# Kernel optimization log

Hardware: AMD Instinct MI355X
Metric: run time of the kernel (lower is better)

## Reference

```python
import jax, jax.numpy as jnp
import numpy as np

# Module hyperparameters (init_kwargs)
NCE_K = 256      # samples per example (col 0 = positive)
NCE_T = 0.07     # temperature
EPS = 1e-7

# Problem sizes
B = 4096         # batch
D = 128          # embedding dim
N = 1_000_000    # memory bank size


def setup_inputs() -> dict:
    key = jax.random.key(0)
    k1, k2, k3, k4 = jax.random.split(key, 4)
    x = jax.random.normal(k1, (B, D), dtype=jnp.float32)
    targets = jax.random.randint(k2, (B,), 0, N)
    memory = jax.random.normal(k3, (N, D), dtype=jnp.float32) * 0.05
    # uniform multinomial-with-replacement sampling == uniform randint
    indices = jax.random.randint(k4, (B, NCE_K), 0, N)
    return {"x": x, "targets": targets, "memory": memory, "indices": indices}


def reference(x, targets, memory, indices):
    # nce_average: overwrite column 0 with the positive index
    idx = indices.at[:, 0].set(targets)              # [B, K]
    weight = memory[idx]                              # [B, K, D] gather
    logits = jnp.einsum('bkd,bd->bk', weight, x) / NCE_T
    sims = jnp.exp(logits)                            # [B, K]
    sims = sims / jnp.sum(sims, axis=1, keepdims=True) * (NCE_K / N)

    # NCE loss: K' = nce_k - 1 noise samples per example
    Kp = NCE_K - 1
    noise = Kp / N
    lnPmt = sims[:, 0] / (sims[:, 0] + noise + EPS)   # [B]
    lnPon = noise / (sims[:, 1:] + noise + EPS)       # [B, K-1]
    loss = -(jnp.log(lnPmt).mean() + jnp.log(lnPon).sum(axis=1).mean())
    return loss
```

## Files before the change

kernel.cpp:

```cpp
#include <hip/hip_runtime.h>

#define B_SZ 4096
#define D_SZ 128
#define K_SZ 256

constexpr float INV_T    = 1.0f / 0.07f;
constexpr float NOISE    = 255.0f / 1000000.0f;
constexpr float EPS_C    = 1e-7f;
constexpr float K_OVER_N = 256.0f / 1000000.0f;

__global__ __launch_bounds__(256, 8) void nce_main(
    const float* __restrict__ x,
    const int*   __restrict__ targets,
    const float* __restrict__ memory,
    const int*   __restrict__ indices,
    float*       __restrict__ partial)
{
    __shared__ float s_e[K_SZ];
    __shared__ float s_red[4];

    const int b    = blockIdx.x;
    const int tid  = threadIdx.x;
    const int lane = tid & 63;
    const int wave = tid >> 6;
    const int sub  = lane & 31;
    const int half = lane >> 5;

    const float4 xv = ((const float4*)(x + (size_t)b * D_SZ))[sub];

    const int myk = wave * 64 + lane;
    const int myidx = (myk == 0) ? targets[b]
                                 : indices[(size_t)b * K_SZ + myk];

    #pragma unroll 4
    for (int it = 0; it < 32; ++it) {
        const int kk  = it * 2 + half;
        const int row = __shfl(myidx, kk, 64);
        const float4 wv = ((const float4*)(memory + (size_t)row * D_SZ))[sub];
        float p = fmaf(wv.x, xv.x, fmaf(wv.y, xv.y,
                  fmaf(wv.z, xv.z, wv.w * xv.w)));
        #pragma unroll
        for (int m = 16; m >= 1; m >>= 1)
            p += __shfl_xor(p, m, 64);
        if (sub == 0)
            s_e[wave * 64 + kk] = expf(p * INV_T);
    }
    __syncthreads();

    const float e = s_e[tid];
    float sum = e;
    #pragma unroll
    for (int m = 32; m >= 1; m >>= 1)
        sum += __shfl_xor(sum, m, 64);
    if (lane == 0) s_red[wave] = sum;
    __syncthreads();
    const float S = s_red[0] + s_red[1] + s_red[2] + s_red[3];

    const float sims = e * (K_OVER_N / S);
    float term;
    if (tid == 0)
        term = logf(sims / (sims + NOISE + EPS_C));
    else
        term = logf(NOISE / (sims + NOISE + EPS_C));

    float t = term;
    #pragma unroll
    for (int m = 32; m >= 1; m >>= 1)
        t += __shfl_xor(t, m, 64);
    __syncthreads();
    if (lane == 0) s_red[wave] = t;
    __syncthreads();
    if (tid == 0)
        partial[b] = s_red[0] + s_red[1] + s_red[2] + s_red[3];
}

__global__ __launch_bounds__(256) void nce_final(
    const float* __restrict__ partial, float* __restrict__ out)
{
    const int tid = threadIdx.x;
    float s = 0.0f;
    #pragma unroll
    for (int i = tid; i < B_SZ; i += 256)
        s += partial[i];
    #pragma unroll
    for (int m = 32; m >= 1; m >>= 1)
        s += __shfl_xor(s, m, 64);
    __shared__ float sr[4];
    if ((tid & 63) == 0) sr[tid >> 6] = s;
    __syncthreads();
    if (tid == 0)
        out[0] = -(sr[0] + sr[1] + sr[2] + sr[3]) / (float)B_SZ;
}

extern "C" void kernel_launch(void* const* d_in, const int* in_sizes, int n_in,
                              void* d_out, int out_size, void* d_ws, size_t ws_size,
                              hipStream_t stream) {
    const float* x       = (const float*)d_in[0];
    const int*   targets = (const int*)  d_in[1];
    const float* memory  = (const float*)d_in[2];
    const int*   indices = (const int*)  d_in[3];
    float* out     = (float*)d_out;
    float* partial = (float*)d_ws;

    nce_main<<<B_SZ, 256, 0, stream>>>(x, targets, memory, indices, partial);
    nce_final<<<1, 256, 0, stream>>>(partial, out);
}
```

Measured before the change: 643.2 us.

## Compute each sampled dot product per thread instead of per half-wave

Remaps work so each of the 256 threads gathers its own memory row and computes the full 128-dim dot product against x staged in shared memory. This removes the per-sample cross-lane shuffle reductions and the shared-memory staging of exponentials. The cost is that each wave-wide load instruction now touches 64 distinct rows, so accesses are uncoalesced and register pressure rises from the fully unrolled loads.

```diff
diff --git a/kernel.cpp b/kernel.cpp
--- a/kernel.cpp
+++ b/kernel.cpp
@@ -16,38 +16,43 @@
     const int*   __restrict__ indices,
     float*       __restrict__ partial)
 {
-    __shared__ float s_e[K_SZ];
-    __shared__ float s_red[4];
+    __shared__ float4 s_x[D_SZ / 4];
+    __shared__ float  s_red[4];
 
     const int b    = blockIdx.x;
     const int tid  = threadIdx.x;
     const int lane = tid & 63;
     const int wave = tid >> 6;
-    const int sub  = lane & 31;
-    const int half = lane >> 5;
 
-    const float4 xv = ((const float4*)(x + (size_t)b * D_SZ))[sub];
+    if (tid < D_SZ / 4)
+        s_x[tid] = ((const float4*)(x + (size_t)b * D_SZ))[tid];
 
-    const int myk = wave * 64 + lane;
-    const int myidx = (myk == 0) ? targets[b]
-                                 : indices[(size_t)b * K_SZ + myk];
-
-    #pragma unroll 4
-    for (int it = 0; it < 32; ++it) {
-        const int kk  = it * 2 + half;
-        const int row = __shfl(myidx, kk, 64);
-        const float4 wv = ((const float4*)(memory + (size_t)row * D_SZ))[sub];
-        float p = fmaf(wv.x, xv.x, fmaf(wv.y, xv.y,
-                  fmaf(wv.z, xv.z, wv.w * xv.w)));
-        #pragma unroll
-        for (int m = 16; m >= 1; m >>= 1)
-            p += __shfl_xor(p, m, 64);
-        if (sub == 0)
-            s_e[wave * 64 + kk] = expf(p * INV_T);
-    }
+    const int myidx = (tid == 0) ? targets[b]
+                                 : indices[(size_t)b * K_SZ + tid];
     __syncthreads();
 
-    const float e = s_e[tid];
+    const float4* __restrict__ wrow =
+        (const float4*)(memory + (size_t)myidx * D_SZ);
+
+    float a0 = 0.f, a1 = 0.f, a2 = 0.f, a3 = 0.f;
+    #pragma unroll
+    for (int j = 0; j < D_SZ / 4; j += 4) {
+        const float4 w0 = wrow[j + 0];
+        const float4 w1 = wrow[j + 1];
+        const float4 w2 = wrow[j + 2];
+        const float4 w3 = wrow[j + 3];
+        const float4 x0 = s_x[j + 0];
+        const float4 x1 = s_x[j + 1];
+        const float4 x2 = s_x[j + 2];
+        const float4 x3 = s_x[j + 3];
+        a0 = fmaf(w0.x, x0.x, fmaf(w0.y, x0.y, fmaf(w0.z, x0.z, fmaf(w0.w, x0.w, a0))));
+        a1 = fmaf(w1.x, x1.x, fmaf(w1.y, x1.y, fmaf(w1.z, x1.z, fmaf(w1.w, x1.w, a1))));
+        a2 = fmaf(w2.x, x2.x, fmaf(w2.y, x2.y, fmaf(w2.z, x2.z, fmaf(w2.w, x2.w, a2))));
+        a3 = fmaf(w3.x, x3.x, fmaf(w3.y, x3.y, fmaf(w3.z, x3.z, fmaf(w3.w, x3.w, a3))));
+    }
+    const float p = (a0 + a1) + (a2 + a3);
+    const float e = expf(p * INV_T);
+
     float sum = e;
     #pragma unroll
     for (int m = 32; m >= 1; m >>= 1)
@@ -57,18 +62,15 @@
     const float S = s_red[0] + s_red[1] + s_red[2] + s_red[3];
 
     const float sims = e * (K_OVER_N / S);
-    float term;
-    if (tid == 0)
-        term = logf(sims / (sims + NOISE + EPS_C));
-    else
-        term = logf(NOISE / (sims + NOISE + EPS_C));
+    float term = (tid == 0)
+        ? logf(sims / (sims + NOISE + EPS_C))
+        : logf(NOISE / (sims + NOISE + EPS_C));
 
-    float t = term;
     #pragma unroll
     for (int m = 32; m >= 1; m >>= 1)
-        t += __shfl_xor(t, m, 64);
+        term += __shfl_xor(term, m, 64);
     __syncthreads();
-    if (lane == 0) s_red[wave] = t;
+    if (lane == 0) s_red[wave] = term;
     __syncthreads();
     if (tid == 0)
         partial[b] = s_red[0] + s_red[1] + s_red[2] + s_red[3];
```

Result: slower. 683.1 us (+6.2%).
